# Performance work log

Hardware: AMD Instinct MI355X
Metric: run time of the kernel (lower is better)

Reference implementation:

```python
import jax, jax.numpy as jnp
import numpy as np

B, H = 32, 1024  # seq_len == hidden_size (required by the original code's shapes)
S = H

def setup_inputs() -> dict:
    key = jax.random.key(0)
    k1, k2, k3, k4, k5 = jax.random.split(key, 5)
    hidden = jax.random.normal(k1, (B, H), dtype=jnp.float32)
    encoder_outputs = jax.random.normal(k2, (B, S, H), dtype=jnp.float32)
    # nn.Linear(2H -> H): weight [H, 2H], bias [H]
    lim = 1.0 / np.sqrt(2 * H)
    W = jax.random.uniform(k3, (H, 2 * H), dtype=jnp.float32, minval=-lim, maxval=lim)
    b = jax.random.uniform(k4, (H,), dtype=jnp.float32, minval=-lim, maxval=lim)
    # v ~ Normal(0, 1/H)
    v = jax.random.normal(k5, (H,), dtype=jnp.float32) * (1.0 / H)
    return {"hidden": hidden, "encoder_outputs": encoder_outputs, "W": W, "b": b, "v": v}

def reference(hidden, encoder_outputs, W, b, v):
    # hidden: [B, H]; encoder_outputs: [B, S, H] with S == H
    S_len = encoder_outputs.shape[1]
    h_rep = jnp.broadcast_to(hidden[:, None, :], (hidden.shape[0], S_len, hidden.shape[1]))
    enc_t = jnp.swapaxes(encoder_outputs, 1, 2)  # [B, H, S] == [B, S, H] (square)
    x = jnp.concatenate([h_rep, enc_t], axis=2)  # [B, S, 2H]
    energy = jnp.tanh(jnp.einsum('bsk,hk->bsh', x, W) + b)  # [B, S, H]
    # scores[b,s] = sum_h v[h] * energy[b,s,h], softmax over s
    scores = jax.nn.softmax(jnp.einsum('h,bsh->bs', v, energy), axis=1)  # [B, S]
    # bmm(scores[B,1,S], enc_t.transpose(1,2)=encoder_outputs[B,S,H]) -> [B, H]
    context = jnp.einsum('bs,bsh->bh', scores, encoder_outputs)
    return context, scores[:, None, :]
```

## Files before the change

### kernel.cpp

```cpp
#include <hip/hip_runtime.h>
#include <hip/hip_bf16.h>
#include <math.h>

#define B_ 32
#define H_ 1024
#define S_ 1024

typedef float  f32x4_t  __attribute__((ext_vector_type(4)));
typedef float  f32x16_t __attribute__((ext_vector_type(16)));
typedef long long i64;
typedef i64 i64x2 __attribute__((ext_vector_type(2)));
typedef unsigned char u8;

__device__ __forceinline__ void gl_lds16(const void* g, void* l) {
    __builtin_amdgcn_global_load_lds(
        (const __attribute__((address_space(1))) unsigned int*)g,
        (__attribute__((address_space(3))) unsigned int*)l, 16, 0, 0);
}

__device__ __forceinline__ float tanh_fast(float x) {
    float e = __builtin_amdgcn_exp2f(x * 2.885390081777927f);
    return 1.f - 2.f * __builtin_amdgcn_rcpf(e + 1.f);
}

__device__ __forceinline__ int kperm(int k) {
    return (k & ~24) | ((k & 8) << 1) | ((k & 16) >> 1);
}

__global__ __launch_bounds__(256) void prep_kernel(
    const float* __restrict__ enc, const float* __restrict__ W,
    const float* __restrict__ hidden, const float* __restrict__ bias,
    u8* __restrict__ encF8, u8* __restrict__ W2f8,
    float* __restrict__ t1, float* __restrict__ logits,
    float* __restrict__ ctx)
{
    const int idx = blockIdx.x;
    const int tid = threadIdx.x;
    if (idx < 4096) {
        const int b   = idx >> 7;
        const int r   = idx & 127;
        const int ktp = r >> 3;
        const int sg  = r & 7;
        const int s   = sg * 128 + (tid >> 1);
        const int c   = tid & 1;
        const float* ebase = enc + (size_t)b * S_ * H_ + s;
        u8* obase = encF8 + (size_t)b * 1048576 + (size_t)s * 32 + c * 16;
        #pragma unroll
        for (int t = 0; t < 2; ++t) {
            const int kt = ktp * 2 + t;
            float f[16];
            #pragma unroll
            for (int i = 0; i < 16; ++i) {
                int k = kt * 32 + 16 * (i >> 3) + 8 * c + (i & 7);
                f[i] = ebase[(size_t)k * H_];
            }
            int w4[4];
            #pragma unroll
            for (int w = 0; w < 4; ++w) {
                int pw = __builtin_amdgcn_cvt_pk_fp8_f32(f[4*w+0], f[4*w+1], 0, false);
                pw     = __builtin_amdgcn_cvt_pk_fp8_f32(f[4*w+2], f[4*w+3], pw, true);
                w4[w] = pw;
            }
            int4 payload = { w4[0], w4[1], w4[2], w4[3] };
            *reinterpret_cast<int4*>(obase + (size_t)kt * 32768) = payload;
        }
    } else if (idx < 5120) {
        int h = idx - 4096;
        if (tid < 64) {
            int z = h * 64 + tid;
            if (z < B_ * S_) logits[z] = 0.f;
            else             ctx[z - B_ * S_] = 0.f;
        }
        int kt = tid >> 3;
        int q  = tid & 7;
        int src = kperm(q * 4);
        float4 wv = *reinterpret_cast<const float4*>(
            W + (size_t)h * (2 * H_) + H_ + kt * 32 + src);
        int pw = __builtin_amdgcn_cvt_pk_fp8_f32(wv.x * 64.f, wv.y * 64.f, 0, false);
        pw     = __builtin_amdgcn_cvt_pk_fp8_f32(wv.z * 64.f, wv.w * 64.f, pw, true);
        *reinterpret_cast<int*>(W2f8 + (size_t)kt * 32768 + (size_t)h * 32 + q * 4) = pw;
    } else {
        int h    = (idx - 5120) * 4 + (tid >> 6);
        int lane = tid & 63;
        const float4* wp = reinterpret_cast<const float4*>(W + (size_t)h * (2 * H_));
        float4 w0 = wp[lane], w1 = wp[lane + 64], w2 = wp[lane + 128], w3 = wp[lane + 192];
        float bh = bias[h];
        for (int b = 0; b < B_; ++b) {
            const float4* hp = reinterpret_cast<const float4*>(hidden + b * H_);
            float4 h0 = hp[lane], h1 = hp[lane + 64], h2 = hp[lane + 128], h3 = hp[lane + 192];
            float a = w0.x*h0.x + w0.y*h0.y + w0.z*h0.z + w0.w*h0.w
                    + w1.x*h1.x + w1.y*h1.y + w1.z*h1.z + w1.w*h1.w
                    + w2.x*h2.x + w2.y*h2.y + w2.z*h2.z + w2.w*h2.w
                    + w3.x*h3.x + w3.y*h3.y + w3.z*h3.z + w3.w*h3.w;
            #pragma unroll
            for (int off = 1; off < 64; off <<= 1) a += __shfl_xor(a, off);
            if (lane == 0) t1[b * H_ + h] = a + bh;
        }
    }
}

__global__ __launch_bounds__(256) void energy_kernel(
    const u8* __restrict__ W2f8, const u8* __restrict__ encF8,
    const float* __restrict__ t1, const float* __restrict__ v,
    float* __restrict__ logits)
{
    __shared__ __align__(16) u8 As[2][2][4096];
    __shared__ __align__(16) u8 Bs[2][2][4096];

    const int id = blockIdx.x;
    const int q  = id >> 3, r = id & 7;
    const int ht = q & 7;
    const int g  = r + ((q >> 3) << 3);
    const int b  = g >> 3;
    const int h0 = ht * 128;
    const int s0 = (g & 7) * 128;

    const int tid   = threadIdx.x;
    const int lane  = tid & 63;
    const int wid   = tid >> 6;
    const int wm    = (wid & 1) * 64;
    const int wn    = (wid >> 1) * 64;
    const int l32   = lane & 31;
    const int khalf = lane >> 5;

    const int rowl = ((lane & 3) << 3) | ((lane >> 2) & 7);
    const int row  = (wid << 5) | rowl;
    const int cch  = lane >> 5;
    const size_t gofsA = (size_t)(h0 + row) * 32 + cch * 16;
    const size_t gofsB = (size_t)b * 1048576 + (size_t)(s0 + row) * 32 + cch * 16;

    gl_lds16(W2f8 + gofsA,          &As[0][0][tid * 16]);
    gl_lds16(W2f8 + gofsA + 32768,  &As[0][1][tid * 16]);
    gl_lds16(encF8 + gofsB,         &Bs[0][0][tid * 16]);
    gl_lds16(encF8 + gofsB + 32768, &Bs[0][1][tid * 16]);
    __syncthreads();

    f32x16_t acc[2][2] = {};
    const int sl  = ((((l32 & 7) << 2) | (l32 >> 3)) | (khalf << 5)) * 16;
    const int wAo = (wm >> 5) * 1024;
    const int wBo = (wn >> 5) * 1024;

    for (int seg = 0; seg < 16; ++seg) {
        const int cur = seg & 1, nxt = cur ^ 1;
        if (seg < 15) {
            const size_t o = (size_t)(2 * seg + 2) * 32768;
            gl_lds16(W2f8 + gofsA + o,          &As[nxt][0][tid * 16]);
            gl_lds16(W2f8 + gofsA + o + 32768,  &As[nxt][1][tid * 16]);
            gl_lds16(encF8 + gofsB + o,         &Bs[nxt][0][tid * 16]);
            gl_lds16(encF8 + gofsB + o + 32768, &Bs[nxt][1][tid * 16]);
        }
        #pragma unroll
        for (int t = 0; t < 2; ++t) {
            i64x2 a0 = *reinterpret_cast<const i64x2*>(&As[cur][t][wAo + sl]);
            i64x2 a1 = *reinterpret_cast<const i64x2*>(&As[cur][t][wAo + 1024 + sl]);
            i64x2 b0 = *reinterpret_cast<const i64x2*>(&Bs[cur][t][wBo + sl]);
            i64x2 b1 = *reinterpret_cast<const i64x2*>(&Bs[cur][t][wBo + 1024 + sl]);
            acc[0][0] = __builtin_amdgcn_mfma_f32_32x32x16_fp8_fp8(a0.x, b0.x, acc[0][0], 0, 0, 0);
            acc[0][1] = __builtin_amdgcn_mfma_f32_32x32x16_fp8_fp8(a0.x, b1.x, acc[0][1], 0, 0, 0);
            acc[1][0] = __builtin_amdgcn_mfma_f32_32x32x16_fp8_fp8(a1.x, b0.x, acc[1][0], 0, 0, 0);
            acc[1][1] = __builtin_amdgcn_mfma_f32_32x32x16_fp8_fp8(a1.x, b1.x, acc[1][1], 0, 0, 0);
            acc[0][0] = __builtin_amdgcn_mfma_f32_32x32x16_fp8_fp8(a0.y, b0.y, acc[0][0], 0, 0, 0);
            acc[0][1] = __builtin_amdgcn_mfma_f32_32x32x16_fp8_fp8(a0.y, b1.y, acc[0][1], 0, 0, 0);
            acc[1][0] = __builtin_amdgcn_mfma_f32_32x32x16_fp8_fp8(a1.y, b0.y, acc[1][0], 0, 0, 0);
            acc[1][1] = __builtin_amdgcn_mfma_f32_32x32x16_fp8_fp8(a1.y, b1.y, acc[1][1], 0, 0, 0);
        }
        __syncthreads();
    }

    float pn0 = 0.f, pn1 = 0.f;
    #pragma unroll
    for (int mt = 0; mt < 2; ++mt)
        #pragma unroll
        for (int rr = 0; rr < 16; ++rr) {
            int rowm = wm + mt * 32 + (rr & 3) + 8 * (rr >> 2) + 4 * khalf;
            int h = h0 + rowm;
            float tv = t1[b * H_ + h];
            float vv = v[h];
            pn0 += vv * tanh_fast(acc[mt][0][rr] * 0.015625f + tv);
            pn1 += vv * tanh_fast(acc[mt][1][rr] * 0.015625f + tv);
        }
    pn0 += __shfl_xor(pn0, 32);
    pn1 += __shfl_xor(pn1, 32);
    if (lane < 32) {
        atomicAdd(&logits[(size_t)b * S_ + s0 + wn + l32], pn0);
        atomicAdd(&logits[(size_t)b * S_ + s0 + wn + 32 + l32], pn1);
    }
}

__global__ __launch_bounds__(256) void ctx_kernel(
    const float* __restrict__ enc, const float* __restrict__ logits,
    float* __restrict__ scores, float* __restrict__ ctx)
{
    __shared__ float sc[1024];
    __shared__ float red[8];
    const int b    = blockIdx.y;
    const int s0   = blockIdx.x * 64;
    const int tid  = threadIdx.x;
    const int lane = tid & 63;
    const int w    = tid >> 6;

    float4 lg = *reinterpret_cast<const float4*>(logits + (size_t)b * S_ + tid * 4);
    float mx = fmaxf(fmaxf(lg.x, lg.y), fmaxf(lg.z, lg.w));
    #pragma unroll
    for (int off = 1; off < 64; off <<= 1) mx = fmaxf(mx, __shfl_xor(mx, off));
    if (lane == 0) red[w] = mx;
    __syncthreads();
    mx = fmaxf(fmaxf(red[0], red[1]), fmaxf(red[2], red[3]));
    const float L2E = 1.44269504088896f;
    float e0 = __builtin_amdgcn_exp2f((lg.x - mx) * L2E);
    float e1 = __builtin_amdgcn_exp2f((lg.y - mx) * L2E);
    float e2 = __builtin_amdgcn_exp2f((lg.z - mx) * L2E);
    float e3 = __builtin_amdgcn_exp2f((lg.w - mx) * L2E);
    float s = e0 + e1 + e2 + e3;
    #pragma unroll
    for (int off = 1; off < 64; off <<= 1) s += __shfl_xor(s, off);
    if (lane == 0) red[4 + w] = s;
    __syncthreads();
    float inv = 1.f / (red[4] + red[5] + red[6] + red[7]);
    float4 sv = { e0 * inv, e1 * inv, e2 * inv, e3 * inv };
    *reinterpret_cast<float4*>(&sc[tid * 4]) = sv;
    if (blockIdx.x == 0)
        *reinterpret_cast<float4*>(scores + (size_t)b * S_ + tid * 4) = sv;
    __syncthreads();

    f32x4_t accv = {0.f, 0.f, 0.f, 0.f};
    const float* ebase = enc + ((size_t)b * S_ + s0) * H_ + tid * 4;
    #pragma unroll 4
    for (int si = 0; si < 64; ++si) {
        float wgt = sc[s0 + si];
        float4 ev = *reinterpret_cast<const float4*>(ebase + (size_t)si * H_);
        accv[0] += wgt * ev.x;
        accv[1] += wgt * ev.y;
        accv[2] += wgt * ev.z;
        accv[3] += wgt * ev.w;
    }
    float* cp = ctx + (size_t)b * H_ + tid * 4;
    atomicAdd(cp + 0, accv[0]);
    atomicAdd(cp + 1, accv[1]);
    atomicAdd(cp + 2, accv[2]);
    atomicAdd(cp + 3, accv[3]);
}

extern "C" void kernel_launch(void* const* d_in, const int* in_sizes, int n_in,
                              void* d_out, int out_size, void* d_ws, size_t ws_size,
                              hipStream_t stream)
{
    (void)in_sizes; (void)n_in; (void)out_size; (void)ws_size;
    const float* hidden = (const float*)d_in[0];
    const float* enc    = (const float*)d_in[1];
    const float* W      = (const float*)d_in[2];
    const float* bias   = (const float*)d_in[3];
    const float* v      = (const float*)d_in[4];

    float* out    = (float*)d_out;
    float* ctx    = out;
    float* scores = out + B_ * H_;

    float* logits = (float*)d_ws;
    float* t1     = logits + B_ * S_;
    u8*    W2f8   = (u8*)(t1 + B_ * H_);
    u8*    encF8  = W2f8 + (size_t)H_ * H_;

    prep_kernel<<<dim3(4096 + 1024 + 256), 256, 0, stream>>>(
        enc, W, hidden, bias, encF8, W2f8, t1, logits, ctx);
    energy_kernel<<<dim3(2048), 256, 0, stream>>>(W2f8, encF8, t1, v, logits);
    ctx_kernel<<<dim3(S_ / 64, B_), 256, 0, stream>>>(enc, logits, scores, ctx);
}
```

Before: 317.3 us.

## Enlarge energy GEMM tiles to 256x256 and vectorize fp8 encoder conversion

The energy GEMM block tile grows from 128x128 to 256x256, so each wave computes a 128x128 sub-tile with a 4x4 accumulator grid. This raises fragment reuse and cuts global and LDS traffic per MFMA, at the cost of higher register pressure, more LDS, and only 512 blocks. The prep kernel's encoder fp8 conversion now reads contiguous float4 rows along s and transposes in registers, replacing strided scalar column loads and using fewer blocks.

```diff
diff --git a/kernel.cpp b/kernel.cpp
--- a/kernel.cpp
+++ b/kernel.cpp
@@ -36,36 +36,37 @@
 {
     const int idx = blockIdx.x;
     const int tid = threadIdx.x;
-    if (idx < 4096) {
-        const int b   = idx >> 7;
-        const int r   = idx & 127;
-        const int ktp = r >> 3;
-        const int sg  = r & 7;
-        const int s   = sg * 128 + (tid >> 1);
-        const int c   = tid & 1;
-        const float* ebase = enc + (size_t)b * S_ * H_ + s;
-        u8* obase = encF8 + (size_t)b * 1048576 + (size_t)s * 32 + c * 16;
-        #pragma unroll
-        for (int t = 0; t < 2; ++t) {
-            const int kt = ktp * 2 + t;
-            float f[16];
-            #pragma unroll
-            for (int i = 0; i < 16; ++i) {
-                int k = kt * 32 + 16 * (i >> 3) + 8 * c + (i & 7);
-                f[i] = ebase[(size_t)k * H_];
+    if (idx < 1024) {
+        const int b  = idx >> 5;
+        const int kt = idx & 31;
+        const int s  = tid * 4;
+        const float* ebase = enc + ((size_t)b * S_ + kt * 32) * H_ + s;
+        f32x4_t L[32];
+        #pragma unroll
+        for (int kk = 0; kk < 32; ++kk)
+            L[kk] = *reinterpret_cast<const f32x4_t*>(ebase + (size_t)kk * H_);
+        u8* obase = encF8 + (size_t)b * 1048576 + (size_t)kt * 32768 + (size_t)s * 32;
+        #pragma unroll
+        for (int jj = 0; jj < 4; ++jj)
+            #pragma unroll
+            for (int c2 = 0; c2 < 2; ++c2) {
+                int w4[4];
+                #pragma unroll
+                for (int w = 0; w < 4; ++w) {
+                    int i0 = 4 * w;
+                    float f0 = L[16 * ((i0 + 0) >> 3) + 8 * c2 + ((i0 + 0) & 7)][jj];
+                    float f1 = L[16 * ((i0 + 1) >> 3) + 8 * c2 + ((i0 + 1) & 7)][jj];
+                    float f2 = L[16 * ((i0 + 2) >> 3) + 8 * c2 + ((i0 + 2) & 7)][jj];
+                    float f3 = L[16 * ((i0 + 3) >> 3) + 8 * c2 + ((i0 + 3) & 7)][jj];
+                    int pw = __builtin_amdgcn_cvt_pk_fp8_f32(f0, f1, 0, false);
+                    pw     = __builtin_amdgcn_cvt_pk_fp8_f32(f2, f3, pw, true);
+                    w4[w] = pw;
+                }
+                int4 payload = { w4[0], w4[1], w4[2], w4[3] };
+                *reinterpret_cast<int4*>(obase + jj * 32 + c2 * 16) = payload;
             }
-            int w4[4];
-            #pragma unroll
-            for (int w = 0; w < 4; ++w) {
-                int pw = __builtin_amdgcn_cvt_pk_fp8_f32(f[4*w+0], f[4*w+1], 0, false);
-                pw     = __builtin_amdgcn_cvt_pk_fp8_f32(f[4*w+2], f[4*w+3], pw, true);
-                w4[w] = pw;
-            }
-            int4 payload = { w4[0], w4[1], w4[2], w4[3] };
-            *reinterpret_cast<int4*>(obase + (size_t)kt * 32768) = payload;
-        }
-    } else if (idx < 5120) {
-        int h = idx - 4096;
+    } else if (idx < 2048) {
+        int h = idx - 1024;
         if (tid < 64) {
             int z = h * 64 + tid;
             if (z < B_ * S_) logits[z] = 0.f;
@@ -80,7 +81,7 @@
         pw     = __builtin_amdgcn_cvt_pk_fp8_f32(wv.z * 64.f, wv.w * 64.f, pw, true);
         *reinterpret_cast<int*>(W2f8 + (size_t)kt * 32768 + (size_t)h * 32 + q * 4) = pw;
     } else {
-        int h    = (idx - 5120) * 4 + (tid >> 6);
+        int h    = (idx - 2048) * 4 + (tid >> 6);
         int lane = tid & 63;
         const float4* wp = reinterpret_cast<const float4*>(W + (size_t)h * (2 * H_));
         float4 w0 = wp[lane], w1 = wp[lane + 64], w2 = wp[lane + 128], w3 = wp[lane + 192];
@@ -99,43 +100,48 @@
     }
 }
 
-__global__ __launch_bounds__(256) void energy_kernel(
+__global__ __launch_bounds__(256, 1) void energy_kernel(
     const u8* __restrict__ W2f8, const u8* __restrict__ encF8,
     const float* __restrict__ t1, const float* __restrict__ v,
     float* __restrict__ logits)
 {
-    __shared__ __align__(16) u8 As[2][2][4096];
-    __shared__ __align__(16) u8 Bs[2][2][4096];
+    __shared__ __align__(16) u8 As[2][2][8192];
+    __shared__ __align__(16) u8 Bs[2][2][8192];
 
     const int id = blockIdx.x;
-    const int q  = id >> 3, r = id & 7;
-    const int ht = q & 7;
-    const int g  = r + ((q >> 3) << 3);
-    const int b  = g >> 3;
-    const int h0 = ht * 128;
-    const int s0 = (g & 7) * 128;
+    const int x  = id & 7, j = id >> 3;
+    const int ht = j & 3;
+    const int G  = x + ((j >> 2) << 3);
+    const int b  = G >> 2;
+    const int h0 = ht * 256;
+    const int s0 = (G & 3) * 256;
 
     const int tid   = threadIdx.x;
     const int lane  = tid & 63;
     const int wid   = tid >> 6;
-    const int wm    = (wid & 1) * 64;
-    const int wn    = (wid >> 1) * 64;
+    const int wm    = (wid & 1) * 128;
+    const int wn    = (wid >> 1) * 128;
     const int l32   = lane & 31;
     const int khalf = lane >> 5;
 
     const int rowl = ((lane & 3) << 3) | ((lane >> 2) & 7);
-    const int row  = (wid << 5) | rowl;
+    const int row0 = ((tid >> 6) << 5) | rowl;
     const int cch  = lane >> 5;
-    const size_t gofsA = (size_t)(h0 + row) * 32 + cch * 16;
-    const size_t gofsB = (size_t)b * 1048576 + (size_t)(s0 + row) * 32 + cch * 16;
-
-    gl_lds16(W2f8 + gofsA,          &As[0][0][tid * 16]);
-    gl_lds16(W2f8 + gofsA + 32768,  &As[0][1][tid * 16]);
-    gl_lds16(encF8 + gofsB,         &Bs[0][0][tid * 16]);
-    gl_lds16(encF8 + gofsB + 32768, &Bs[0][1][tid * 16]);
-    __syncthreads();
-
-    f32x16_t acc[2][2] = {};
+    const size_t gA0 = (size_t)(h0 + row0) * 32 + cch * 16;
+    const size_t gA1 = gA0 + 128 * 32;
+    const size_t gB0 = (size_t)b * 1048576 + (size_t)(s0 + row0) * 32 + cch * 16;
+    const size_t gB1 = gB0 + 128 * 32;
+
+    #pragma unroll
+    for (int ktl = 0; ktl < 2; ++ktl) {
+        gl_lds16(W2f8 + gA0 + ktl * 32768,  &As[0][ktl][tid * 16]);
+        gl_lds16(W2f8 + gA1 + ktl * 32768,  &As[0][ktl][4096 + tid * 16]);
+        gl_lds16(encF8 + gB0 + ktl * 32768, &Bs[0][ktl][tid * 16]);
+        gl_lds16(encF8 + gB1 + ktl * 32768, &Bs[0][ktl][4096 + tid * 16]);
+    }
+    __syncthreads();
+
+    f32x16_t acc[4][4] = {};
     const int sl  = ((((l32 & 7) << 2) | (l32 >> 3)) | (khalf << 5)) * 16;
     const int wAo = (wm >> 5) * 1024;
     const int wBo = (wn >> 5) * 1024;
@@ -144,46 +150,54 @@
         const int cur = seg & 1, nxt = cur ^ 1;
         if (seg < 15) {
             const size_t o = (size_t)(2 * seg + 2) * 32768;
-            gl_lds16(W2f8 + gofsA + o,          &As[nxt][0][tid * 16]);
-            gl_lds16(W2f8 + gofsA + o + 32768,  &As[nxt][1][tid * 16]);
-            gl_lds16(encF8 + gofsB + o,         &Bs[nxt][0][tid * 16]);
-            gl_lds16(encF8 + gofsB + o + 32768, &Bs[nxt][1][tid * 16]);
-        }
-        #pragma unroll
-        for (int t = 0; t < 2; ++t) {
-            i64x2 a0 = *reinterpret_cast<const i64x2*>(&As[cur][t][wAo + sl]);
-            i64x2 a1 = *reinterpret_cast<const i64x2*>(&As[cur][t][wAo + 1024 + sl]);
-            i64x2 b0 = *reinterpret_cast<const i64x2*>(&Bs[cur][t][wBo + sl]);
-            i64x2 b1 = *reinterpret_cast<const i64x2*>(&Bs[cur][t][wBo + 1024 + sl]);
-            acc[0][0] = __builtin_amdgcn_mfma_f32_32x32x16_fp8_fp8(a0.x, b0.x, acc[0][0], 0, 0, 0);
-            acc[0][1] = __builtin_amdgcn_mfma_f32_32x32x16_fp8_fp8(a0.x, b1.x, acc[0][1], 0, 0, 0);
-            acc[1][0] = __builtin_amdgcn_mfma_f32_32x32x16_fp8_fp8(a1.x, b0.x, acc[1][0], 0, 0, 0);
-            acc[1][1] = __builtin_amdgcn_mfma_f32_32x32x16_fp8_fp8(a1.x, b1.x, acc[1][1], 0, 0, 0);
-            acc[0][0] = __builtin_amdgcn_mfma_f32_32x32x16_fp8_fp8(a0.y, b0.y, acc[0][0], 0, 0, 0);
-            acc[0][1] = __builtin_amdgcn_mfma_f32_32x32x16_fp8_fp8(a0.y, b1.y, acc[0][1], 0, 0, 0);
-            acc[1][0] = __builtin_amdgcn_mfma_f32_32x32x16_fp8_fp8(a1.y, b0.y, acc[1][0], 0, 0, 0);
-            acc[1][1] = __builtin_amdgcn_mfma_f32_32x32x16_fp8_fp8(a1.y, b1.y, acc[1][1], 0, 0, 0);
+            #pragma unroll
+            for (int ktl = 0; ktl < 2; ++ktl) {
+                gl_lds16(W2f8 + gA0 + o + ktl * 32768,  &As[nxt][ktl][tid * 16]);
+                gl_lds16(W2f8 + gA1 + o + ktl * 32768,  &As[nxt][ktl][4096 + tid * 16]);
+                gl_lds16(encF8 + gB0 + o + ktl * 32768, &Bs[nxt][ktl][tid * 16]);
+                gl_lds16(encF8 + gB1 + o + ktl * 32768, &Bs[nxt][ktl][4096 + tid * 16]);
+            }
+        }
+        #pragma unroll
+        for (int ktl = 0; ktl < 2; ++ktl) {
+            i64x2 af[4], bf[4];
+            #pragma unroll
+            for (int mt = 0; mt < 4; ++mt)
+                af[mt] = *reinterpret_cast<const i64x2*>(&As[cur][ktl][wAo + mt * 1024 + sl]);
+            #pragma unroll
+            for (int nt = 0; nt < 4; ++nt)
+                bf[nt] = *reinterpret_cast<const i64x2*>(&Bs[cur][ktl][wBo + nt * 1024 + sl]);
+            #pragma unroll
+            for (int mt = 0; mt < 4; ++mt)
+                #pragma unroll
+                for (int nt = 0; nt < 4; ++nt) {
+                    acc[mt][nt] = __builtin_amdgcn_mfma_f32_32x32x16_fp8_fp8(
+                        af[mt].x, bf[nt].x, acc[mt][nt], 0, 0, 0);
+                    acc[mt][nt] = __builtin_amdgcn_mfma_f32_32x32x16_fp8_fp8(
+                        af[mt].y, bf[nt].y, acc[mt][nt], 0, 0, 0);
+                }
         }
         __syncthreads();
     }
 
-    float pn0 = 0.f, pn1 = 0.f;
-    #pragma unroll
-    for (int mt = 0; mt < 2; ++mt)
+    float pn[4] = {0.f, 0.f, 0.f, 0.f};
+    #pragma unroll
+    for (int mt = 0; mt < 4; ++mt)
         #pragma unroll
         for (int rr = 0; rr < 16; ++rr) {
             int rowm = wm + mt * 32 + (rr & 3) + 8 * (rr >> 2) + 4 * khalf;
             int h = h0 + rowm;
             float tv = t1[b * H_ + h];
             float vv = v[h];
-            pn0 += vv * tanh_fast(acc[mt][0][rr] * 0.015625f + tv);
-            pn1 += vv * tanh_fast(acc[mt][1][rr] * 0.015625f + tv);
-        }
-    pn0 += __shfl_xor(pn0, 32);
-    pn1 += __shfl_xor(pn1, 32);
-    if (lane < 32) {
-        atomicAdd(&logits[(size_t)b * S_ + s0 + wn + l32], pn0);
-        atomicAdd(&logits[(size_t)b * S_ + s0 + wn + 32 + l32], pn1);
+            #pragma unroll
+            for (int nt = 0; nt < 4; ++nt)
+                pn[nt] += vv * tanh_fast(acc[mt][nt][rr] * 0.015625f + tv);
+        }
+    #pragma unroll
+    for (int nt = 0; nt < 4; ++nt) {
+        pn[nt] += __shfl_xor(pn[nt], 32);
+        if (lane < 32)
+            atomicAdd(&logits[(size_t)b * S_ + s0 + wn + nt * 32 + l32], pn[nt]);
     }
 }
 
@@ -261,8 +275,8 @@
     u8*    W2f8   = (u8*)(t1 + B_ * H_);
     u8*    encF8  = W2f8 + (size_t)H_ * H_;
 
-    prep_kernel<<<dim3(4096 + 1024 + 256), 256, 0, stream>>>(
+    prep_kernel<<<dim3(1024 + 1024 + 256), 256, 0, stream>>>(
         enc, W, hidden, bias, encF8, W2f8, t1, logits, ctx);
-    energy_kernel<<<dim3(2048), 256, 0, stream>>>(W2f8, encF8, t1, v, logits);
+    energy_kernel<<<dim3(512), 256, 0, stream>>>(W2f8, encF8, t1, v, logits);
     ctx_kernel<<<dim3(S_ / 64, B_), 256, 0, stream>>>(enc, logits, scores, ctx);
 }
```

Measured after the change: 338.7 us. 6.7% more time.

## Coalesce encoder FP8 transpose-pack loads and split context reduction finer

Applied to the files above, without the earlier changes.

The encoder FP8 packing stage now has each thread load 32 rows of float4 vectors, which gives fully coalesced 16-byte reads. It then packs four sequence positions per thread from registers, replacing the old strided scalar loads. The number of prep blocks drops from 4096 to 1024, so each thread holds many more registers. Separately, the context kernel now covers 16 sequence positions per block instead of 64. This gives four times as many blocks for more parallelism, at the cost of more atomics and redundant softmax work per block.

```diff
diff --git a/kernel.cpp b/kernel.cpp
--- a/kernel.cpp
+++ b/kernel.cpp
@@ -36,36 +36,37 @@
 {
     const int idx = blockIdx.x;
     const int tid = threadIdx.x;
-    if (idx < 4096) {
-        const int b   = idx >> 7;
-        const int r   = idx & 127;
-        const int ktp = r >> 3;
-        const int sg  = r & 7;
-        const int s   = sg * 128 + (tid >> 1);
-        const int c   = tid & 1;
-        const float* ebase = enc + (size_t)b * S_ * H_ + s;
-        u8* obase = encF8 + (size_t)b * 1048576 + (size_t)s * 32 + c * 16;
-        #pragma unroll
-        for (int t = 0; t < 2; ++t) {
-            const int kt = ktp * 2 + t;
-            float f[16];
+    if (idx < 1024) {
+        const int b  = idx >> 5;
+        const int kt = idx & 31;
+        const int s  = tid * 4;
+        const float* ebase = enc + ((size_t)b * S_ + kt * 32) * H_ + s;
+        f32x4_t L[32];
+        #pragma unroll
+        for (int kk = 0; kk < 32; ++kk)
+            L[kk] = *reinterpret_cast<const f32x4_t*>(ebase + (size_t)kk * H_);
+        u8* obase = encF8 + (size_t)b * 1048576 + (size_t)kt * 32768 + (size_t)s * 32;
+        #pragma unroll
+        for (int jj = 0; jj < 4; ++jj)
             #pragma unroll
-            for (int i = 0; i < 16; ++i) {
-                int k = kt * 32 + 16 * (i >> 3) + 8 * c + (i & 7);
-                f[i] = ebase[(size_t)k * H_];
+            for (int c2 = 0; c2 < 2; ++c2) {
+                int w4[4];
+                #pragma unroll
+                for (int w = 0; w < 4; ++w) {
+                    int i0 = 4 * w;
+                    float f0 = L[16 * ((i0 + 0) >> 3) + 8 * c2 + ((i0 + 0) & 7)][jj];
+                    float f1 = L[16 * ((i0 + 1) >> 3) + 8 * c2 + ((i0 + 1) & 7)][jj];
+                    float f2 = L[16 * ((i0 + 2) >> 3) + 8 * c2 + ((i0 + 2) & 7)][jj];
+                    float f3 = L[16 * ((i0 + 3) >> 3) + 8 * c2 + ((i0 + 3) & 7)][jj];
+                    int pw = __builtin_amdgcn_cvt_pk_fp8_f32(f0, f1, 0, false);
+                    pw     = __builtin_amdgcn_cvt_pk_fp8_f32(f2, f3, pw, true);
+                    w4[w] = pw;
+                }
+                int4 payload = { w4[0], w4[1], w4[2], w4[3] };
+                *reinterpret_cast<int4*>(obase + jj * 32 + c2 * 16) = payload;
             }
-            int w4[4];
-            #pragma unroll
-            for (int w = 0; w < 4; ++w) {
-                int pw = __builtin_amdgcn_cvt_pk_fp8_f32(f[4*w+0], f[4*w+1], 0, false);
-                pw     = __builtin_amdgcn_cvt_pk_fp8_f32(f[4*w+2], f[4*w+3], pw, true);
-                w4[w] = pw;
-            }
-            int4 payload = { w4[0], w4[1], w4[2], w4[3] };
-            *reinterpret_cast<int4*>(obase + (size_t)kt * 32768) = payload;
-        }
-    } else if (idx < 5120) {
-        int h = idx - 4096;
+    } else if (idx < 2048) {
+        int h = idx - 1024;
         if (tid < 64) {
             int z = h * 64 + tid;
             if (z < B_ * S_) logits[z] = 0.f;
@@ -80,7 +81,7 @@
         pw     = __builtin_amdgcn_cvt_pk_fp8_f32(wv.z * 64.f, wv.w * 64.f, pw, true);
         *reinterpret_cast<int*>(W2f8 + (size_t)kt * 32768 + (size_t)h * 32 + q * 4) = pw;
     } else {
-        int h    = (idx - 5120) * 4 + (tid >> 6);
+        int h    = (idx - 2048) * 4 + (tid >> 6);
         int lane = tid & 63;
         const float4* wp = reinterpret_cast<const float4*>(W + (size_t)h * (2 * H_));
         float4 w0 = wp[lane], w1 = wp[lane + 64], w2 = wp[lane + 128], w3 = wp[lane + 192];
@@ -194,7 +195,7 @@
     __shared__ float sc[1024];
     __shared__ float red[8];
     const int b    = blockIdx.y;
-    const int s0   = blockIdx.x * 64;
+    const int s0   = blockIdx.x * 16;
     const int tid  = threadIdx.x;
     const int lane = tid & 63;
     const int w    = tid >> 6;
@@ -225,8 +226,8 @@
 
     f32x4_t accv = {0.f, 0.f, 0.f, 0.f};
     const float* ebase = enc + ((size_t)b * S_ + s0) * H_ + tid * 4;
-    #pragma unroll 4
-    for (int si = 0; si < 64; ++si) {
+    #pragma unroll
+    for (int si = 0; si < 16; ++si) {
         float wgt = sc[s0 + si];
         float4 ev = *reinterpret_cast<const float4*>(ebase + (size_t)si * H_);
         accv[0] += wgt * ev.x;
@@ -261,8 +262,8 @@
     u8*    W2f8   = (u8*)(t1 + B_ * H_);
     u8*    encF8  = W2f8 + (size_t)H_ * H_;
 
-    prep_kernel<<<dim3(4096 + 1024 + 256), 256, 0, stream>>>(
+    prep_kernel<<<dim3(1024 + 1024 + 256), 256, 0, stream>>>(
         enc, W, hidden, bias, encF8, W2f8, t1, logits, ctx);
     energy_kernel<<<dim3(2048), 256, 0, stream>>>(W2f8, encF8, t1, v, logits);
-    ctx_kernel<<<dim3(S_ / 64, B_), 256, 0, stream>>>(enc, logits, scores, ctx);
-}
+    ctx_kernel<<<dim3(S_ / 16, B_), 256, 0, stream>>>(enc, logits, scores, ctx);
+}
```

Result: slower. 342.3 us (+7.9%).
